# Performance work log

Hardware: AMD Instinct MI355X
Metric: run time of the kernel (lower is better)

The kernel has to match this reference:

```python
import jax, jax.numpy as jnp
import numpy as np

B, N, C = 4, 3136, 64
IMG_H = IMG_W = 56
HEADS = 1
TOPK = 8
HID = 4 * C  # mlp_ratio=4.0


def _ln(x, g, b, eps=1e-5):
    m = x.mean(-1, keepdims=True)
    v = ((x - m) ** 2).mean(-1, keepdims=True)
    return (x - m) * jax.lax.rsqrt(v + eps) * g + b


def _conv(x, w, b, pad, groups):
    y = jax.lax.conv_general_dilated(
        x, w, (1, 1), [(pad, pad), (pad, pad)],
        dimension_numbers=('NCHW', 'OIHW', 'NCHW'), feature_group_count=groups)
    return y + b[None, :, None, None]


def setup_inputs() -> dict:
    key = jax.random.key(0)
    ks = jax.random.split(key, 10)
    def rn(k, shp, scale=0.02):
        return jax.random.normal(k, shp, jnp.float32) * scale
    return {
        'x': jax.random.normal(ks[0], (B, N, C), jnp.float32),
        'norm1_g': jnp.ones((C,), jnp.float32), 'norm1_b': jnp.zeros((C,), jnp.float32),
        'wq': rn(ks[1], (C, C)), 'bq': jnp.zeros((C,), jnp.float32),
        'wkv': rn(ks[2], (C, 2 * C)), 'bkv': jnp.zeros((2 * C,), jnp.float32),
        'wproj': rn(ks[3], (C, C)), 'bproj': jnp.zeros((C,), jnp.float32),
        'local_w': rn(ks[4], (C, C // HEADS, 3, 3), 0.05), 'local_b': jnp.zeros((C,), jnp.float32),
        'norm2_g': jnp.ones((C,), jnp.float32), 'norm2_b': jnp.zeros((C,), jnp.float32),
        'w3': rn(ks[5], (HID, 1, 3, 3), 0.05), 'b3': jnp.zeros((HID,), jnp.float32),
        'w5': rn(ks[6], (HID, 1, 5, 5), 0.05), 'b5': jnp.zeros((HID,), jnp.float32),
        'w1': rn(ks[7], (C, 2 * HID, 1, 1), 0.05), 'b1': jnp.zeros((C,), jnp.float32),
        'H': IMG_H, 'W': IMG_W,
    }


def reference(x, norm1_g, norm1_b, wq, bq, wkv, bkv, wproj, bproj,
              local_w, local_b, norm2_g, norm2_b, w3, b3, w5, b5, w1, b1, H, W):
    Bb, Nn, Cc = x.shape
    d = Cc // HEADS
    scale = d ** -0.5
    # --- DynamicSparseAttention (global branch) ---
    xn = _ln(x, norm1_g, norm1_b)
    q = (xn @ wq + bq).reshape(Bb, Nn, HEADS, d).transpose(0, 2, 1, 3)       # bhnd
    kv = (xn @ wkv + bkv).reshape(Bb, Nn, 2, HEADS, d)
    k = kv[:, :, 0].transpose(0, 2, 1, 3)
    v = kv[:, :, 1].transpose(0, 2, 1, 3)
    attn = jnp.einsum('bhnd,bhmd->bhnm', q, k) * scale                        # [B,h,N,N]
    kth = jax.lax.top_k(attn, TOPK)[0][..., -1:]                              # k-th largest per row
    mask = (attn >= kth).astype(attn.dtype)                                   # top-k scatter mask
    p = jax.nn.softmax(attn * mask, axis=-1)                                  # zeros kept (as in torch ref)
    g = jnp.einsum('bhnm,bhmd->bhnd', p, v).transpose(0, 2, 1, 3).reshape(Bb, Nn, Cc)
    g = g @ wproj + bproj
    # --- local conv attention branch ---
    x_img = x.transpose(0, 2, 1).reshape(Bb, Cc, H, W)
    loc = _conv(x_img, local_w, local_b, 1, HEADS).reshape(Bb, Cc, Nn).transpose(0, 2, 1)
    # --- residual 1 (note: norm1 params reused, as in source) ---
    x = x + _ln(g + loc, norm1_g, norm1_b)
    # --- MSFN ---
    xn2 = _ln(x, norm2_g, norm2_b).transpose(0, 2, 1).reshape(Bb, Cc, H, W)
    x3 = _conv(xn2, w3, b3, 1, Cc)   # depthwise 3x3, channel mult 4
    x5 = _conv(xn2, w5, b5, 2, Cc)   # depthwise 5x5, channel mult 4
    m = _conv(jnp.concatenate([x3, x5], axis=1), w1, b1, 0, 1)
    return x + m.reshape(Bb, Cc, Nn).transpose(0, 2, 1)
```

## Files before the change

### kernel.cpp

```cpp
#include <hip/hip_runtime.h>
#include <math.h>

#define Bv 4
#define Nv 3136
#define Cv 64
#define Hh 56
#define Ww 56
#define HIDv 256
#define TOPKv 8
#define TSP 520
#define LCP 584
#define XNP 72

constexpr float SCALE = 0.125f;
constexpr float EPS = 1e-5f;

typedef short bf16x8 __attribute__((ext_vector_type(8)));
typedef float f32x4 __attribute__((ext_vector_type(4)));

#define CSWAP(a, b) { unsigned int _hi = max(a, b); unsigned int _lo = min(a, b); a = _hi; b = _lo; }
#define BITONIC8(T) \
  CSWAP(T[0], T[4]); CSWAP(T[1], T[5]); CSWAP(T[2], T[6]); CSWAP(T[3], T[7]); \
  CSWAP(T[0], T[2]); CSWAP(T[1], T[3]); CSWAP(T[4], T[6]); CSWAP(T[5], T[7]); \
  CSWAP(T[0], T[1]); CSWAP(T[2], T[3]); CSWAP(T[4], T[5]); CSWAP(T[6], T[7]);

__device__ __forceinline__ unsigned short f2bf(float f) {
  unsigned int u = __float_as_uint(f);
  u = (u + 0x7FFFu + ((u >> 16) & 1u)) >> 16;
  return (unsigned short)u;
}
__device__ __forceinline__ float bf2f(unsigned short u) {
  return __uint_as_float(((unsigned int)u) << 16);
}
__device__ __forceinline__ unsigned int pack2(float a, float b) {
  return (unsigned int)f2bf(a) | ((unsigned int)f2bf(b) << 16);
}

__device__ __forceinline__ unsigned int packScore(float s, int j) {
  unsigned int b = __float_as_uint(s);
  unsigned int m = b ^ ((b & 0x80000000u) ? 0xFFFFFFFFu : 0x80000000u);
  return (m & 0xFFFFF000u) | (unsigned int)j;
}
__device__ __forceinline__ float unpackScore(unsigned int p) {
  unsigned int m = p & 0xFFFFF000u;
  unsigned int b = (m & 0x80000000u) ? (m ^ 0x80000000u) : ~m;
  return __uint_as_float(b);
}

__global__ void k_transpose(const float* __restrict__ w1, const float* __restrict__ lw,
                            const float* __restrict__ w3, const float* __restrict__ w5,
                            const float* __restrict__ wq, const float* __restrict__ wkv,
                            const float* __restrict__ bq, const float* __restrict__ bkv,
                            const float* __restrict__ wproj,
                            unsigned short* __restrict__ w1bf, unsigned short* __restrict__ lwb,
                            float* __restrict__ w3t, float* __restrict__ w5t,
                            unsigned short* __restrict__ wqkvt, float* __restrict__ qkvb,
                            unsigned short* __restrict__ wprojt) {
  int p = blockIdx.x * 256 + threadIdx.x;
  if (p < 64 * 512) w1bf[p] = f2bf(w1[p]);
  if (p < 64 * 576) {
    int co = p / 576, k = p % 576;
    int tap = k >> 6, ci = k & 63;
    lwb[p] = f2bf(lw[co * 576 + ci * 9 + tap]);
  }
  if (p < 36 * 64) {
    int cin = p & 63, tm = p >> 6;
    int tap = tm >> 2, m = tm & 3;
    w3t[p] = w3[(cin * 4 + m) * 9 + tap];
  }
  if (p < 100 * 64) {
    int cin = p & 63, tm = p >> 6;
    int tap = tm >> 2, m = tm & 3;
    w5t[p] = w5[(cin * 4 + m) * 25 + tap];
  }
  if (p < 192 * 64) {
    int o = p >> 6, i = p & 63;
    float v = (o < 64) ? wq[i * 64 + o] : wkv[i * 128 + (o - 64)];
    wqkvt[p] = f2bf(v);
  }
  if (p < 192) qkvb[p] = (p < 64) ? bq[p] : bkv[p - 64];
  if (p < 64 * 64) {
    int o = p >> 6, i = p & 63;
    wprojt[p] = f2bf(wproj[i * 64 + o]);
  }
}

__global__ __launch_bounds__(256) void k_ln_qkv(
    const float* __restrict__ x, const float* __restrict__ g1, const float* __restrict__ b1,
    const unsigned short* __restrict__ wqkvt, const float* __restrict__ qkvb,
    unsigned short* __restrict__ q16, unsigned short* __restrict__ k16,
    float* __restrict__ vo, unsigned short* __restrict__ x16,
    float* __restrict__ sumv) {
  __shared__ __align__(16) unsigned short xnS[16 * XNP];
  int bid = blockIdx.x;
  int b = bid / 196, tile = bid % 196;
  size_t tok0 = (size_t)b * Nv + tile * 16;
  int t = threadIdx.x;
  int w = t >> 6, l = t & 63;
  int tokL = t >> 4;
  int ch0 = (t & 15) * 4;
  size_t tok = tok0 + tokL;
  float v[4];
  *(float4*)v = *(const float4*)&x[tok * 64 + ch0];
  {
    unsigned int pk[2] = {pack2(v[0], v[1]), pack2(v[2], v[3])};
    *(uint2*)&x16[tok * 64 + ch0] = *(uint2*)pk;
  }
  float s = v[0] + v[1] + v[2] + v[3];
  float s2 = v[0] * v[0] + v[1] * v[1] + v[2] * v[2] + v[3] * v[3];
#pragma unroll
  for (int off = 1; off <= 8; off <<= 1) {
    s += __shfl_xor(s, off, 64);
    s2 += __shfl_xor(s2, off, 64);
  }
  float m = s * (1.f / 64.f);
  float rs = rsqrtf(s2 * (1.f / 64.f) - m * m + EPS);
  {
    unsigned int pk[2];
    float a0_ = (v[0] - m) * rs * g1[ch0] + b1[ch0];
    float a1_ = (v[1] - m) * rs * g1[ch0 + 1] + b1[ch0 + 1];
    float a2_ = (v[2] - m) * rs * g1[ch0 + 2] + b1[ch0 + 2];
    float a3_ = (v[3] - m) * rs * g1[ch0 + 3] + b1[ch0 + 3];
    pk[0] = pack2(a0_, a1_);
    pk[1] = pack2(a2_, a3_);
    *(uint2*)&xnS[tokL * XNP + ch0] = *(uint2*)pk;
  }
  __syncthreads();
  int n = l & 15, q = l >> 4;
  const bf16x8 a0 = *(const bf16x8*)&xnS[n * XNP + q * 8];
  const bf16x8 a1 = *(const bf16x8*)&xnS[n * XNP + 32 + q * 8];
  {
    const unsigned short* wr = &wqkvt[(size_t)(w * 16 + n) * 64];
    bf16x8 b0 = *(const bf16x8*)&wr[q * 8];
    bf16x8 b1_ = *(const bf16x8*)&wr[32 + q * 8];
    f32x4 acc = {0.f, 0.f, 0.f, 0.f};
    acc = __builtin_amdgcn_mfma_f32_16x16x32_bf16(a0, b0, acc, 0, 0, 0);
    acc = __builtin_amdgcn_mfma_f32_16x16x32_bf16(a1, b1_, acc, 0, 0, 0);
    float bias = qkvb[w * 16 + n];
#pragma unroll
    for (int r = 0; r < 4; ++r)
      q16[(tok0 + q * 4 + r) * 64 + w * 16 + n] = f2bf(acc[r] + bias);
  }
  {
    const unsigned short* wr = &wqkvt[(size_t)((w + 4) * 16 + n) * 64];
    bf16x8 b0 = *(const bf16x8*)&wr[q * 8];
    bf16x8 b1_ = *(const bf16x8*)&wr[32 + q * 8];
    f32x4 acc = {0.f, 0.f, 0.f, 0.f};
    acc = __builtin_amdgcn_mfma_f32_16x16x32_bf16(a0, b0, acc, 0, 0, 0);
    acc = __builtin_amdgcn_mfma_f32_16x16x32_bf16(a1, b1_, acc, 0, 0, 0);
    float bias = qkvb[64 + w * 16 + n];
#pragma unroll
    for (int r = 0; r < 4; ++r)
      k16[(tok0 + q * 4 + r) * 64 + w * 16 + n] = f2bf(acc[r] + bias);
  }
  {
    const unsigned short* wr = &wqkvt[(size_t)((w + 8) * 16 + n) * 64];
    bf16x8 b0 = *(const bf16x8*)&wr[q * 8];
    bf16x8 b1_ = *(const bf16x8*)&wr[32 + q * 8];
    f32x4 acc = {0.f, 0.f, 0.f, 0.f};
    acc = __builtin_amdgcn_mfma_f32_16x16x32_bf16(a0, b0, acc, 0, 0, 0);
    acc = __builtin_amdgcn_mfma_f32_16x16x32_bf16(a1, b1_, acc, 0, 0, 0);
    float bias = qkvb[128 + w * 16 + n];
    float vp = acc[0] + acc[1] + acc[2] + acc[3] + 4.0f * bias;
#pragma unroll
    for (int r = 0; r < 4; ++r)
      vo[(tok0 + q * 4 + r) * 64 + w * 16 + n] = acc[r] + bias;
    vp += __shfl_xor(vp, 16, 64);
    vp += __shfl_xor(vp, 32, 64);
    if (q == 0) atomicAdd(&sumv[b * 64 + w * 16 + n], vp);
  }
}

__global__ __launch_bounds__(256) void k_attn_topk(
    const unsigned short* __restrict__ q16, const unsigned short* __restrict__ k16,
    unsigned int* __restrict__ top8out) {
  __shared__ unsigned int candLDS[16][4][9];
  int bid = blockIdx.x;
  int quarter = bid & 3;
  int lin = bid >> 2;
  int b = lin / 196, tile = lin % 196;
  int qbase = b * Nv + tile * 16;
  size_t bN = (size_t)b * Nv;
  int t = threadIdx.x;
  int w = t >> 6, lane = t & 63;
  int qcol = lane & 15, quad = lane >> 4;

  const bf16x8 qf0 = *(const bf16x8*)&q16[((size_t)(qbase + qcol)) * 64 + quad * 8];
  const bf16x8 qf1 = *(const bf16x8*)&q16[((size_t)(qbase + qcol)) * 64 + 32 + quad * 8];

  unsigned int t8a[8], t8b[8];
  unsigned int PACKNEG = packScore(-1e30f, 0);
#pragma unroll
  for (int u = 0; u < 8; ++u) { t8a[u] = PACKNEG; t8b[u] = PACKNEG; }

  int chBeg = (quarter * 49) >> 2;
  int chEnd = ((quarter + 1) * 49) >> 2;
  int nch = chEnd - chBeg;
  int keyRow = w * 16 + qcol;
  const unsigned short* kbase = &k16[(bN + (size_t)chBeg * 64 + keyRow) * 64];

  bf16x8 ka0 = *(const bf16x8*)&kbase[quad * 8];
  bf16x8 ka1 = *(const bf16x8*)&kbase[32 + quad * 8];
  bf16x8 kb0 = *(const bf16x8*)&kbase[(size_t)64 * 64 + quad * 8];
  bf16x8 kb1 = *(const bf16x8*)&kbase[(size_t)64 * 64 + 32 + quad * 8];

#pragma unroll 1
  for (int i = 0; i + 1 < nch; i += 2) {
    bf16x8 ca0 = ka0, ca1 = ka1, cb0 = kb0, cb1 = kb1;
    int ia = min(i + 2, nch - 1), ib = min(i + 3, nch - 1);
    ka0 = *(const bf16x8*)&kbase[(size_t)ia * 4096 + quad * 8];
    ka1 = *(const bf16x8*)&kbase[(size_t)ia * 4096 + 32 + quad * 8];
    kb0 = *(const bf16x8*)&kbase[(size_t)ib * 4096 + quad * 8];
    kb1 = *(const bf16x8*)&kbase[(size_t)ib * 4096 + 32 + quad * 8];

    f32x4 accA = {0.f, 0.f, 0.f, 0.f};
    accA = __builtin_amdgcn_mfma_f32_16x16x32_bf16(ca0, qf0, accA, 0, 0, 0);
    accA = __builtin_amdgcn_mfma_f32_16x16x32_bf16(ca1, qf1, accA, 0, 0, 0);
    f32x4 accB = {0.f, 0.f, 0.f, 0.f};
    accB = __builtin_amdgcn_mfma_f32_16x16x32_bf16(cb0, qf0, accB, 0, 0, 0);
    accB = __builtin_amdgcn_mfma_f32_16x16x32_bf16(cb1, qf1, accB, 0, 0, 0);

    {
      int jb = (chBeg + i) * 64 + w * 16 + quad * 4;
      unsigned int p0 = packScore(accA[0], jb + 0);
      unsigned int p1 = packScore(accA[1], jb + 1);
      unsigned int p2 = packScore(accA[2], jb + 2);
      unsigned int p3 = packScore(accA[3], jb + 3);
      CSWAP(p0, p1); CSWAP(p2, p3); CSWAP(p0, p2); CSWAP(p1, p3); CSWAP(p1, p2);
      t8a[4] = max(t8a[4], p3);
      t8a[5] = max(t8a[5], p2);
      t8a[6] = max(t8a[6], p1);
      t8a[7] = max(t8a[7], p0);
      BITONIC8(t8a);
    }
    {
      int jb = (chBeg + i + 1) * 64 + w * 16 + quad * 4;
      unsigned int p0 = packScore(accB[0], jb + 0);
      unsigned int p1 = packScore(accB[1], jb + 1);
      unsigned int p2 = packScore(accB[2], jb + 2);
      unsigned int p3 = packScore(accB[3], jb + 3);
      CSWAP(p0, p1); CSWAP(p2, p3); CSWAP(p0, p2); CSWAP(p1, p3); CSWAP(p1, p2);
      t8b[4] = max(t8b[4], p3);
      t8b[5] = max(t8b[5], p2);
      t8b[6] = max(t8b[6], p1);
      t8b[7] = max(t8b[7], p0);
      BITONIC8(t8b);
    }
  }
  if (nch & 1) {
    f32x4 accA = {0.f, 0.f, 0.f, 0.f};
    accA = __builtin_amdgcn_mfma_f32_16x16x32_bf16(ka0, qf0, accA, 0, 0, 0);
    accA = __builtin_amdgcn_mfma_f32_16x16x32_bf16(ka1, qf1, accA, 0, 0, 0);
    int jb = (chEnd - 1) * 64 + w * 16 + quad * 4;
    unsigned int p0 = packScore(accA[0], jb + 0);
    unsigned int p1 = packScore(accA[1], jb + 1);
    unsigned int p2 = packScore(accA[2], jb + 2);
    unsigned int p3 = packScore(accA[3], jb + 3);
    CSWAP(p0, p1); CSWAP(p2, p3); CSWAP(p0, p2); CSWAP(p1, p3); CSWAP(p1, p2);
    t8a[4] = max(t8a[4], p3);
    t8a[5] = max(t8a[5], p2);
    t8a[6] = max(t8a[6], p1);
    t8a[7] = max(t8a[7], p0);
    BITONIC8(t8a);
  }

  unsigned int t8[8];
#pragma unroll
  for (int i = 0; i < 8; ++i) t8[i] = max(t8a[i], t8b[7 - i]);
  BITONIC8(t8);

#pragma unroll
  for (int step = 16; step <= 32; step <<= 1) {
    unsigned int o[8];
#pragma unroll
    for (int i = 0; i < 8; ++i) o[i] = (unsigned int)__shfl_xor((int)t8[i], step, 64);
    unsigned int nw[8];
#pragma unroll
    for (int i = 0; i < 8; ++i) nw[i] = max(t8[i], o[7 - i]);
#pragma unroll
    for (int i = 0; i < 8; ++i) t8[i] = nw[i];
    BITONIC8(t8);
  }
  if (quad == 0) {
#pragma unroll
    for (int i = 0; i < 8; ++i) candLDS[qcol][w][i] = t8[i];
  }
  __syncthreads();

  if (t < 16) {
    int r = t;
    int p0 = 0, p1 = 0, p2 = 0, p3 = 0;
    size_t obase = ((size_t)(bN + tile * 16 + r)) * 32 + quarter * 8;
#pragma unroll
    for (int u = 0; u < 8; ++u) {
      unsigned int c0 = (p0 < 8) ? candLDS[r][0][p0] : 0u;
      unsigned int c1 = (p1 < 8) ? candLDS[r][1][p1] : 0u;
      unsigned int c2 = (p2 < 8) ? candLDS[r][2][p2] : 0u;
      unsigned int c3 = (p3 < 8) ? candLDS[r][3][p3] : 0u;
      unsigned int best = c0;
      int bw = 0;
      if (c1 > best) { best = c1; bw = 1; }
      if (c2 > best) { best = c2; bw = 2; }
      if (c3 > best) { best = c3; bw = 3; }
      p0 += (bw == 0); p1 += (bw == 1); p2 += (bw == 2); p3 += (bw == 3);
      top8out[obase + u] = best;
    }
  }
}

__global__ __launch_bounds__(256) void k_attn_proj(
    const unsigned int* __restrict__ top8, const float* __restrict__ vg,
    const float* __restrict__ sumv,
    const float* __restrict__ x, const float* __restrict__ loc,
    const unsigned short* __restrict__ wprojt, const float* __restrict__ bproj,
    const float* __restrict__ g1, const float* __restrict__ b1,
    const float* __restrict__ g2, const float* __restrict__ b2,
    float* __restrict__ x2, unsigned short* __restrict__ xn2b) {
  __shared__ float kwS[16][8];
  __shared__ int kidxS[16][8];
  __shared__ float invZS[16];
  __shared__ __align__(16) unsigned short gS[16 * XNP];
  __shared__ float yS[16 * 66];
  int bid = blockIdx.x;
  int b = bid / 196, tile = bid % 196;
  size_t bN = (size_t)b * Nv;
  size_t tok0 = bN + tile * 16;
  int t = threadIdx.x;
  if (t < 16) {
    size_t base = (tok0 + t) * 32;
    unsigned int A[8];
#pragma unroll
    for (int i = 0; i < 8; ++i) A[i] = top8[base + i];
#pragma unroll
    for (int h = 1; h < 4; ++h) {
      unsigned int Bb[8];
#pragma unroll
      for (int i = 0; i < 8; ++i) Bb[i] = top8[base + h * 8 + i];
#pragma unroll
      for (int i = 0; i < 8; ++i) A[i] = max(A[i], Bb[7 - i]);
      BITONIC8(A);
    }
    float Z = (float)(Nv - TOPKv);
#pragma unroll
    for (int u = 0; u < 8; ++u) {
      float s = unpackScore(A[u]) * SCALE;
      float e = __expf(s);
      kwS[t][u] = e - 1.0f;
      kidxS[t][u] = (int)(A[u] & 0xFFFu);
      Z += e;
    }
    invZS[t] = 1.0f / Z;
  }
  __syncthreads();
  {
    int c = t & 63, rg = t >> 6;
    float sv = sumv[b * 64 + c];
#pragma unroll
    for (int rr = 0; rr < 4; ++rr) {
      int tokL = rg * 4 + rr;
      float acc = sv;
#pragma unroll
      for (int u = 0; u < 8; ++u)
        acc += kwS[tokL][u] * vg[(bN + kidxS[tokL][u]) * 64 + c];
      gS[tokL * XNP + c] = f2bf(acc * invZS[tokL]);
    }
  }
  __syncthreads();
  int w = t >> 6, l = t & 63;
  int n = l & 15, q = l >> 4;
  {
    const bf16x8 a0 = *(const bf16x8*)&gS[n * XNP + q * 8];
    const bf16x8 a1 = *(const bf16x8*)&gS[n * XNP + 32 + q * 8];
    const unsigned short* wr = &wprojt[(size_t)(w * 16 + n) * 64];
    bf16x8 b0 = *(const bf16x8*)&wr[q * 8];
    bf16x8 b1_ = *(const bf16x8*)&wr[32 + q * 8];
    f32x4 acc = {0.f, 0.f, 0.f, 0.f};
    acc = __builtin_amdgcn_mfma_f32_16x16x32_bf16(a0, b0, acc, 0, 0, 0);
    acc = __builtin_amdgcn_mfma_f32_16x16x32_bf16(a1, b1_, acc, 0, 0, 0);
    float bias = bproj[w * 16 + n];
#pragma unroll
    for (int r = 0; r < 4; ++r) {
      size_t idx = (tok0 + q * 4 + r) * 64 + w * 16 + n;
      yS[(q * 4 + r) * 66 + w * 16 + n] = acc[r] + bias + loc[idx];
    }
  }
  __syncthreads();
  int tokL = t >> 4;
  int ch0 = (t & 15) * 4;
  size_t tok = tok0 + tokL;
  float y[4];
#pragma unroll
  for (int i = 0; i < 4; ++i) y[i] = yS[tokL * 66 + ch0 + i];
  float s = y[0] + y[1] + y[2] + y[3];
  float s2 = y[0] * y[0] + y[1] * y[1] + y[2] * y[2] + y[3] * y[3];
#pragma unroll
  for (int off = 1; off <= 8; off <<= 1) {
    s += __shfl_xor(s, off, 64);
    s2 += __shfl_xor(s2, off, 64);
  }
  float m1 = s * (1.f / 64.f);
  float rs1 = rsqrtf(s2 * (1.f / 64.f) - m1 * m1 + EPS);
  float xv[4];
  *(float4*)xv = *(const float4*)&x[tok * 64 + ch0];
  float x2v[4];
  float t_s = 0.f, t_s2 = 0.f;
#pragma unroll
  for (int i = 0; i < 4; ++i) {
    float t1 = (y[i] - m1) * rs1 * g1[ch0 + i] + b1[ch0 + i];
    x2v[i] = xv[i] + t1;
    t_s += x2v[i];
    t_s2 += x2v[i] * x2v[i];
  }
#pragma unroll
  for (int off = 1; off <= 8; off <<= 1) {
    t_s += __shfl_xor(t_s, off, 64);
    t_s2 += __shfl_xor(t_s2, off, 64);
  }
  float m2 = t_s * (1.f / 64.f);
  float rs2 = rsqrtf(t_s2 * (1.f / 64.f) - m2 * m2 + EPS);
  *(float4*)&x2[tok * 64 + ch0] = *(float4*)x2v;
  unsigned int pk[2];
  {
    float a0_ = (x2v[0] - m2) * rs2 * g2[ch0] + b2[ch0];
    float a1_ = (x2v[1] - m2) * rs2 * g2[ch0 + 1] + b2[ch0 + 1];
    float a2_ = (x2v[2] - m2) * rs2 * g2[ch0 + 2] + b2[ch0 + 2];
    float a3_ = (x2v[3] - m2) * rs2 * g2[ch0 + 3] + b2[ch0 + 3];
    pk[0] = pack2(a0_, a1_);
    pk[1] = pack2(a2_, a3_);
  }
  *(uint2*)&xn2b[tok * 64 + ch0] = *(uint2*)pk;
}

__global__ __launch_bounds__(256) void k_locconv(
    const unsigned short* __restrict__ x16, const unsigned short* __restrict__ lwb,
    const float* __restrict__ lb, float* __restrict__ loc) {
  __shared__ __align__(16) unsigned short im[16 * LCP];
  int bid = blockIdx.x;
  int b = bid / 196, rem = bid % 196;
  int th = rem / 7, tw = rem % 7;
  int h0 = th * 2, w0 = tw * 8;
  size_t bN = (size_t)b * Nv;
  int t = threadIdx.x;
  for (int p = t; p < 1152; p += 256) {
    int sub = p & 7, s = p >> 3;
    int tok = s / 9, tap = s % 9;
    int tr = tok >> 3, tc = tok & 7;
    int dh = tap / 3, dw = tap % 3;
    int gh = h0 + tr - 1 + dh, gw = w0 + tc - 1 + dw;
    bf16x8 v = {};
    if (gh >= 0 && gh < Hh && gw >= 0 && gw < Ww)
      v = *(const bf16x8*)&x16[(bN + gh * Ww + gw) * 64 + sub * 8];
    *(bf16x8*)&im[tok * LCP + tap * 64 + sub * 8] = v;
  }
  __syncthreads();
  int wv = t >> 6, lane = t & 63;
  int n16 = lane & 15, quad = lane >> 4;
  const unsigned short* wrow = &lwb[(size_t)(wv * 16 + n16) * 576];
  f32x4 acc = {0.f, 0.f, 0.f, 0.f};
#pragma unroll 6
  for (int kk = 0; kk < 18; ++kk) {
    bf16x8 af = *(const bf16x8*)&im[n16 * LCP + kk * 32 + quad * 8];
    bf16x8 bfr = *(const bf16x8*)&wrow[kk * 32 + quad * 8];
    acc = __builtin_amdgcn_mfma_f32_16x16x32_bf16(af, bfr, acc, 0, 0, 0);
  }
  float bias = lb[wv * 16 + n16];
#pragma unroll
  for (int r = 0; r < 4; ++r) {
    int tok = quad * 4 + r;
    int trr = tok >> 3, tcc = tok & 7;
    size_t idx = (bN + (size_t)(h0 + trr) * Ww + w0 + tcc) * 64 + wv * 16 + n16;
    loc[idx] = acc[r] + bias;
  }
}

__global__ __launch_bounds__(256) void k_msfn(
    const unsigned short* __restrict__ xn2b, const float* __restrict__ x2,
    const float* __restrict__ w3t, const float* __restrict__ b3,
    const float* __restrict__ w5t, const float* __restrict__ b5,
    const unsigned short* __restrict__ w1bf, const float* __restrict__ b1,
    float* __restrict__ out) {
  __shared__ __align__(16) unsigned short xtS[6 * 12 * 64];
  __shared__ __align__(16) unsigned short tsS[16 * TSP];

  int bid = blockIdx.x;
  int b = bid / 196;
  int rem = bid % 196;
  int th = rem / 7, tw = rem % 7;
  int h0 = th * 2, w0 = tw * 8;
  size_t bN = (size_t)b * Nv;
  int t = threadIdx.x;

  unsigned int* xtU = (unsigned int*)xtS;
  for (int p = t; p < 6 * 12 * 32; p += 256) {
    int cp = p & 31, rc = p >> 5;
    int r = rc / 12, cc = rc % 12;
    int gh = h0 - 2 + r, gw = w0 - 2 + cc;
    unsigned int v = 0;
    if (gh >= 0 && gh < Hh && gw >= 0 && gw < Ww)
      v = *(const unsigned int*)&xn2b[(bN + gh * Ww + gw) * 64 + cp * 2];
    xtU[rc * 32 + cp] = v;
  }
  __syncthreads();

  int cin = t & 63, tg = t >> 6;
  int tr = tg >> 1, tc0 = (tg & 1) * 4;
  float win[5][8];
#pragma unroll
  for (int r = 0; r < 5; ++r)
#pragma unroll
    for (int c = 0; c < 8; ++c)
      win[r][c] = bf2f(xtS[((tr + r) * 12 + tc0 + c) * 64 + cin]);

  unsigned int* tsU = (unsigned int*)tsS;
#pragma unroll 1
  for (int m2 = 0; m2 < 4; m2 += 2) {
    float a3[2][9], a5[2][25], bb3[2], bb5[2];
#pragma unroll
    for (int mm = 0; mm < 2; ++mm) {
      int m = m2 + mm;
#pragma unroll
      for (int tap = 0; tap < 9; ++tap) a3[mm][tap] = w3t[(tap * 4 + m) * 64 + cin];
#pragma unroll
      for (int tap = 0; tap < 25; ++tap) a5[mm][tap] = w5t[(tap * 4 + m) * 64 + cin];
      bb3[mm] = b3[cin * 4 + m];
      bb5[mm] = b5[cin * 4 + m];
    }
#pragma unroll
    for (int tk = 0; tk < 4; ++tk) {
      int tok = tg * 4 + tk;
      unsigned int p3 = 0, p5 = 0;
#pragma unroll
      for (int mm = 0; mm < 2; ++mm) {
        float acc3 = bb3[mm];
#pragma unroll
        for (int kh = 0; kh < 3; ++kh)
#pragma unroll
          for (int kw2 = 0; kw2 < 3; ++kw2)
            acc3 += win[1 + kh][tk + 1 + kw2] * a3[mm][kh * 3 + kw2];
        float acc5 = bb5[mm];
#pragma unroll
        for (int kh = 0; kh < 5; ++kh)
#pragma unroll
          for (int kw2 = 0; kw2 < 5; ++kw2)
            acc5 += win[kh][tk + kw2] * a5[mm][kh * 5 + kw2];
        p3 |= (unsigned int)f2bf(acc3) << (16 * mm);
        p5 |= (unsigned int)f2bf(acc5) << (16 * mm);
      }
      tsU[(tok * TSP + cin * 4 + m2) >> 1] = p3;
      tsU[(tok * TSP + 256 + cin * 4 + m2) >> 1] = p5;
    }
  }
  __syncthreads();

  int wv = tg, lane = t & 63;
  int n16 = lane & 15, quad = lane >> 4;
  const unsigned short* wrow = &w1bf[(size_t)(wv * 16 + n16) * 512];
  f32x4 acc = {0.f, 0.f, 0.f, 0.f};
#pragma unroll 4
  for (int kk = 0; kk < 16; ++kk) {
    bf16x8 af = *(const bf16x8*)&tsS[n16 * TSP + kk * 32 + quad * 8];
    bf16x8 bfr = *(const bf16x8*)&wrow[kk * 32 + quad * 8];
    acc = __builtin_amdgcn_mfma_f32_16x16x32_bf16(af, bfr, acc, 0, 0, 0);
  }
  float bias = b1[wv * 16 + n16];
#pragma unroll
  for (int r = 0; r < 4; ++r) {
    int tok = quad * 4 + r;
    int trr = tok >> 3, tcc = tok & 7;
    size_t idx = (bN + (size_t)(h0 + trr) * Ww + w0 + tcc) * 64 + wv * 16 + n16;
    out[idx] = x2[idx] + acc[r] + bias;
  }
}

extern "C" void kernel_launch(void* const* d_in, const int* in_sizes, int n_in,
                              void* d_out, int out_size, void* d_ws, size_t ws_size,
                              hipStream_t stream) {
  const float* x = (const float*)d_in[0];
  const float* n1g = (const float*)d_in[1];
  const float* n1b = (const float*)d_in[2];
  const float* wq = (const float*)d_in[3];
  const float* bq = (const float*)d_in[4];
  const float* wkv = (const float*)d_in[5];
  const float* bkv = (const float*)d_in[6];
  const float* wproj = (const float*)d_in[7];
  const float* bproj = (const float*)d_in[8];
  const float* lw = (const float*)d_in[9];
  const float* lb = (const float*)d_in[10];
  const float* n2g = (const float*)d_in[11];
  const float* n2b = (const float*)d_in[12];
  const float* w3 = (const float*)d_in[13];
  const float* b3 = (const float*)d_in[14];
  const float* w5 = (const float*)d_in[15];
  const float* b5 = (const float*)d_in[16];
  const float* w1 = (const float*)d_in[17];
  const float* b1 = (const float*)d_in[18];
  float* out = (float*)d_out;

  float* ws = (float*)d_ws;
  const size_t TOK = (size_t)Bv * Nv * Cv;
  float* vb = ws;
  float* sumv = vb + TOK;
  float* loc = sumv + 256;
  float* x2 = loc + TOK;
  float* w3t = x2 + TOK;
  float* w5t = w3t + 2304;
  float* qkvb = w5t + 6400;
  unsigned short* q16 = (unsigned short*)(qkvb + 192);
  unsigned short* k16 = q16 + TOK;
  unsigned short* xn2b = k16 + TOK;
  unsigned short* x16 = xn2b + TOK;
  unsigned short* w1bf = x16 + TOK;
  unsigned short* lwb = w1bf + 64 * 512;
  unsigned short* wqkvt = lwb + 64 * 576;
  unsigned short* wprojt = wqkvt + 192 * 64;
  unsigned int* top8ws = (unsigned int*)(wprojt + 64 * 64 + 64);

  hipMemsetAsync(sumv, 0, 256 * sizeof(float), stream);
  k_transpose<<<144, 256, 0, stream>>>(w1, lw, w3, w5, wq, wkv, bq, bkv, wproj,
                                       w1bf, lwb, w3t, w5t, wqkvt, qkvb, wprojt);
  k_ln_qkv<<<Bv * 196, 256, 0, stream>>>(x, n1g, n1b, wqkvt, qkvb, q16, k16, vb, x16, sumv);
  k_attn_topk<<<Bv * 196 * 4, 256, 0, stream>>>(q16, k16, top8ws);
  k_locconv<<<Bv * 196, 256, 0, stream>>>(x16, lwb, lb, loc);
  k_attn_proj<<<Bv * 196, 256, 0, stream>>>(top8ws, vb, sumv, x, loc, wprojt, bproj,
                                            n1g, n1b, n2g, n2b, x2, xn2b);
  k_msfn<<<Bv * 196, 256, 0, stream>>>(xn2b, x2, w3t, b3, w5t, b5, w1bf, b1, out);
}
```

Measured before the change: 191.9 us.

## Fuse local 3x3 conv into attention projection kernel, drop loc and x16 buffers

The local conv (im2col plus MFMA) moves into k_attn_proj, which now tiles tokens as 2x8 spatial patches and builds the im2col directly from fp32 x. This removes a kernel launch, the fp32 loc round trip through global memory, and the bf16 x16 copy written by k_ln_qkv. In exchange the fused kernel uses more LDS (an extra ~18KB im2col tile), which may reduce occupancy, and it reads fp32 x, which doubles the bytes loaded for the im2col gather.

```diff
diff --git a/kernel.cpp b/kernel.cpp
--- a/kernel.cpp
+++ b/kernel.cpp
@@ -89,8 +89,7 @@
     const float* __restrict__ x, const float* __restrict__ g1, const float* __restrict__ b1,
     const unsigned short* __restrict__ wqkvt, const float* __restrict__ qkvb,
     unsigned short* __restrict__ q16, unsigned short* __restrict__ k16,
-    float* __restrict__ vo, unsigned short* __restrict__ x16,
-    float* __restrict__ sumv) {
+    float* __restrict__ vo, float* __restrict__ sumv) {
   __shared__ __align__(16) unsigned short xnS[16 * XNP];
   int bid = blockIdx.x;
   int b = bid / 196, tile = bid % 196;
@@ -102,10 +101,6 @@
   size_t tok = tok0 + tokL;
   float v[4];
   *(float4*)v = *(const float4*)&x[tok * 64 + ch0];
-  {
-    unsigned int pk[2] = {pack2(v[0], v[1]), pack2(v[2], v[3])};
-    *(uint2*)&x16[tok * 64 + ch0] = *(uint2*)pk;
-  }
   float s = v[0] + v[1] + v[2] + v[3];
   float s2 = v[0] * v[0] + v[1] * v[1] + v[2] * v[2] + v[3] * v[3];
 #pragma unroll
@@ -310,8 +305,8 @@
 
 __global__ __launch_bounds__(256) void k_attn_proj(
     const unsigned int* __restrict__ top8, const float* __restrict__ vg,
-    const float* __restrict__ sumv,
-    const float* __restrict__ x, const float* __restrict__ loc,
+    const float* __restrict__ sumv, const float* __restrict__ x,
+    const unsigned short* __restrict__ lwb, const float* __restrict__ lb,
     const unsigned short* __restrict__ wprojt, const float* __restrict__ bproj,
     const float* __restrict__ g1, const float* __restrict__ b1,
     const float* __restrict__ g2, const float* __restrict__ b2,
@@ -319,15 +314,38 @@
   __shared__ float kwS[16][8];
   __shared__ int kidxS[16][8];
   __shared__ float invZS[16];
+  __shared__ __align__(16) unsigned short imS[16 * LCP];
   __shared__ __align__(16) unsigned short gS[16 * XNP];
   __shared__ float yS[16 * 66];
   int bid = blockIdx.x;
-  int b = bid / 196, tile = bid % 196;
+  int b = bid / 196, rem = bid % 196;
+  int th = rem / 7, tw = rem % 7;
+  int h0 = th * 2, w0 = tw * 8;
   size_t bN = (size_t)b * Nv;
-  size_t tok0 = bN + tile * 16;
   int t = threadIdx.x;
+
+  for (int p = t; p < 1152; p += 256) {
+    int sub = p & 7, s = p >> 3;
+    int tok = s / 9, tap = s % 9;
+    int tr = tok >> 3, tc = tok & 7;
+    int dh = tap / 3, dw = tap % 3;
+    int gh = h0 + tr - 1 + dh, gw = w0 + tc - 1 + dw;
+    uint4 uu = {0u, 0u, 0u, 0u};
+    if (gh >= 0 && gh < Hh && gw >= 0 && gw < Ww) {
+      const float* xp = &x[(bN + gh * Ww + gw) * 64 + sub * 8];
+      float4 va = *(const float4*)xp;
+      float4 vb = *(const float4*)(xp + 4);
+      uu.x = pack2(va.x, va.y);
+      uu.y = pack2(va.z, va.w);
+      uu.z = pack2(vb.x, vb.y);
+      uu.w = pack2(vb.z, vb.w);
+    }
+    *(uint4*)&imS[tok * LCP + tap * 64 + sub * 8] = uu;
+  }
+
   if (t < 16) {
-    size_t base = (tok0 + t) * 32;
+    int gtok = (h0 + (t >> 3)) * Ww + w0 + (t & 7);
+    size_t base = (bN + gtok) * 32;
     unsigned int A[8];
 #pragma unroll
     for (int i = 0; i < 8; ++i) A[i] = top8[base + i];
@@ -352,6 +370,22 @@
     invZS[t] = 1.0f / Z;
   }
   __syncthreads();
+
+  int w = t >> 6, l = t & 63;
+  int n = l & 15, q = l >> 4;
+
+  f32x4 lacc = {0.f, 0.f, 0.f, 0.f};
+  {
+    const unsigned short* lwrow = &lwb[(size_t)(w * 16 + n) * 576];
+#pragma unroll 6
+    for (int kk = 0; kk < 18; ++kk) {
+      bf16x8 af = *(const bf16x8*)&imS[n * LCP + kk * 32 + q * 8];
+      bf16x8 bfr = *(const bf16x8*)&lwrow[kk * 32 + q * 8];
+      lacc = __builtin_amdgcn_mfma_f32_16x16x32_bf16(af, bfr, lacc, 0, 0, 0);
+    }
+  }
+  float lbias = lb[w * 16 + n];
+
   {
     int c = t & 63, rg = t >> 6;
     float sv = sumv[b * 64 + c];
@@ -366,8 +400,7 @@
     }
   }
   __syncthreads();
-  int w = t >> 6, l = t & 63;
-  int n = l & 15, q = l >> 4;
+
   {
     const bf16x8 a0 = *(const bf16x8*)&gS[n * XNP + q * 8];
     const bf16x8 a1 = *(const bf16x8*)&gS[n * XNP + 32 + q * 8];
@@ -379,15 +412,14 @@
     acc = __builtin_amdgcn_mfma_f32_16x16x32_bf16(a1, b1_, acc, 0, 0, 0);
     float bias = bproj[w * 16 + n];
 #pragma unroll
-    for (int r = 0; r < 4; ++r) {
-      size_t idx = (tok0 + q * 4 + r) * 64 + w * 16 + n;
-      yS[(q * 4 + r) * 66 + w * 16 + n] = acc[r] + bias + loc[idx];
-    }
+    for (int r = 0; r < 4; ++r)
+      yS[(q * 4 + r) * 66 + w * 16 + n] = acc[r] + bias + lacc[r] + lbias;
   }
   __syncthreads();
+
   int tokL = t >> 4;
   int ch0 = (t & 15) * 4;
-  size_t tok = tok0 + tokL;
+  size_t tok = bN + (size_t)(h0 + (tokL >> 3)) * Ww + w0 + (tokL & 7);
   float y[4];
 #pragma unroll
   for (int i = 0; i < 4; ++i) y[i] = yS[tokL * 66 + ch0 + i];
@@ -429,48 +461,6 @@
     pk[1] = pack2(a2_, a3_);
   }
   *(uint2*)&xn2b[tok * 64 + ch0] = *(uint2*)pk;
-}
-
-__global__ __launch_bounds__(256) void k_locconv(
-    const unsigned short* __restrict__ x16, const unsigned short* __restrict__ lwb,
-    const float* __restrict__ lb, float* __restrict__ loc) {
-  __shared__ __align__(16) unsigned short im[16 * LCP];
-  int bid = blockIdx.x;
-  int b = bid / 196, rem = bid % 196;
-  int th = rem / 7, tw = rem % 7;
-  int h0 = th * 2, w0 = tw * 8;
-  size_t bN = (size_t)b * Nv;
-  int t = threadIdx.x;
-  for (int p = t; p < 1152; p += 256) {
-    int sub = p & 7, s = p >> 3;
-    int tok = s / 9, tap = s % 9;
-    int tr = tok >> 3, tc = tok & 7;
-    int dh = tap / 3, dw = tap % 3;
-    int gh = h0 + tr - 1 + dh, gw = w0 + tc - 1 + dw;
-    bf16x8 v = {};
-    if (gh >= 0 && gh < Hh && gw >= 0 && gw < Ww)
-      v = *(const bf16x8*)&x16[(bN + gh * Ww + gw) * 64 + sub * 8];
-    *(bf16x8*)&im[tok * LCP + tap * 64 + sub * 8] = v;
-  }
-  __syncthreads();
-  int wv = t >> 6, lane = t & 63;
-  int n16 = lane & 15, quad = lane >> 4;
-  const unsigned short* wrow = &lwb[(size_t)(wv * 16 + n16) * 576];
-  f32x4 acc = {0.f, 0.f, 0.f, 0.f};
-#pragma unroll 6
-  for (int kk = 0; kk < 18; ++kk) {
-    bf16x8 af = *(const bf16x8*)&im[n16 * LCP + kk * 32 + quad * 8];
-    bf16x8 bfr = *(const bf16x8*)&wrow[kk * 32 + quad * 8];
-    acc = __builtin_amdgcn_mfma_f32_16x16x32_bf16(af, bfr, acc, 0, 0, 0);
-  }
-  float bias = lb[wv * 16 + n16];
-#pragma unroll
-  for (int r = 0; r < 4; ++r) {
-    int tok = quad * 4 + r;
-    int trr = tok >> 3, tcc = tok & 7;
-    size_t idx = (bN + (size_t)(h0 + trr) * Ww + w0 + tcc) * 64 + wv * 16 + n16;
-    loc[idx] = acc[r] + bias;
-  }
 }
 
 __global__ __launch_bounds__(256) void k_msfn(
@@ -600,16 +590,14 @@
   const size_t TOK = (size_t)Bv * Nv * Cv;
   float* vb = ws;
   float* sumv = vb + TOK;
-  float* loc = sumv + 256;
-  float* x2 = loc + TOK;
+  float* x2 = sumv + 256;
   float* w3t = x2 + TOK;
   float* w5t = w3t + 2304;
   float* qkvb = w5t + 6400;
   unsigned short* q16 = (unsigned short*)(qkvb + 192);
   unsigned short* k16 = q16 + TOK;
   unsigned short* xn2b = k16 + TOK;
-  unsigned short* x16 = xn2b + TOK;
-  unsigned short* w1bf = x16 + TOK;
+  unsigned short* w1bf = xn2b + TOK;
   unsigned short* lwb = w1bf + 64 * 512;
   unsigned short* wqkvt = lwb + 64 * 576;
   unsigned short* wprojt = wqkvt + 192 * 64;
@@ -618,10 +606,9 @@
   hipMemsetAsync(sumv, 0, 256 * sizeof(float), stream);
   k_transpose<<<144, 256, 0, stream>>>(w1, lw, w3, w5, wq, wkv, bq, bkv, wproj,
                                        w1bf, lwb, w3t, w5t, wqkvt, qkvb, wprojt);
-  k_ln_qkv<<<Bv * 196, 256, 0, stream>>>(x, n1g, n1b, wqkvt, qkvb, q16, k16, vb, x16, sumv);
+  k_ln_qkv<<<Bv * 196, 256, 0, stream>>>(x, n1g, n1b, wqkvt, qkvb, q16, k16, vb, sumv);
   k_attn_topk<<<Bv * 196 * 4, 256, 0, stream>>>(q16, k16, top8ws);
-  k_locconv<<<Bv * 196, 256, 0, stream>>>(x16, lwb, lb, loc);
-  k_attn_proj<<<Bv * 196, 256, 0, stream>>>(top8ws, vb, sumv, x, loc, wprojt, bproj,
+  k_attn_proj<<<Bv * 196, 256, 0, stream>>>(top8ws, vb, sumv, x, lwb, lb, wprojt, bproj,
                                             n1g, n1b, n2g, n2b, x2, xn2b);
   k_msfn<<<Bv * 196, 256, 0, stream>>>(xn2b, x2, w3t, b3, w5t, b5, w1bf, b1, out);
 }
```

Result: no change. 192.8 us (+0.5%).
